# Kernel tuning notes

Measured on AMD Instinct MI355X. Metric: run time of the kernel, lower is better.

The kernel has to match this reference:

```python
import math
import jax, jax.numpy as jnp
import numpy as np

B, T_ALL, D = 128, 197, 768
T = T_ALL - 1
ORG, E, DFF, NCLS = 5, 8, 1024, 100
CAP_FACTOR = 1.25
MAX_K = 2  # training=True -> min(2, n_experts)


def setup_inputs() -> dict:
    key = jax.random.key(0)
    ks = jax.random.split(key, 16)
    s = lambda *sh: 0.02
    inp = {
        "tokens": jax.random.normal(ks[0], (B, T_ALL, D), jnp.float32),
        "organ_priors": jax.random.uniform(ks[1], (B, ORG), jnp.float32),
        "router_w": jax.random.normal(ks[2], (D + ORG, E), jnp.float32) * 0.02,
        "router_b": jnp.zeros((E,), jnp.float32),
        "w1": jax.random.normal(ks[3], (E, D, DFF), jnp.float32) * 0.02,
        "b1": jnp.zeros((E, DFF), jnp.float32),
        "w2": jax.random.normal(ks[4], (E, DFF, D), jnp.float32) * 0.02,
        "b2": jnp.zeros((E, D), jnp.float32),
        "ln_g": jnp.ones((D,), jnp.float32),
        "ln_b": jnp.zeros((D,), jnp.float32),
        "cls_w": jax.random.normal(ks[5], (D, NCLS), jnp.float32) * 0.02,
        "cls_b": jnp.zeros((NCLS,), jnp.float32),
        "aux_w": jax.random.normal(ks[6], (D, ORG), jnp.float32) * 0.02,
        "aux_b": jnp.zeros((ORG,), jnp.float32),
    }
    return inp


def switch_moe(flat, flat_prior, router_w, router_b, w1, b1, w2, b2):
    N = flat.shape[0]
    capacity = math.ceil(N / E * CAP_FACTOR)  # static
    logits = jnp.concatenate([flat, flat_prior], axis=-1) @ router_w + router_b  # (N,E)
    probs = jax.nn.softmax(logits, axis=-1)
    entropy = -(probs * jnp.log(probs + 1e-12)).sum(-1)  # (N,)
    topk_vals, topk_idx = jax.lax.top_k(probs, MAX_K)  # (N,K)
    topk_probs = topk_vals / (topk_vals.sum(-1, keepdims=True) + 1e-12)
    # one-hot expert assignment over top-k slots: (N,E)
    sel = jnp.any(topk_idx[:, None, :] == jnp.arange(E)[None, :, None], axis=-1)
    # combine weight per (token, expert): first (unique) matching top-k slot's prob
    w_full = (topk_probs[:, None, :] * (topk_idx[:, None, :] == jnp.arange(E)[None, :, None])).sum(-1)  # (N,E)
    # capacity-limited dispatch: per expert keep top-`capacity` tokens by router prob
    score = jnp.where(sel, probs, -jnp.inf).T  # (E,N)
    top_scores, idx = jax.lax.top_k(score, capacity)  # (E,cap), sorted desc like torch.sort
    valid = jnp.isfinite(top_scores)  # (E,cap)
    gathered = flat[idx]  # (E,cap,D)
    h = jax.nn.gelu(jnp.einsum('ecd,edf->ecf', gathered, w1) + b1[:, None, :], approximate=False)
    out_sel = jnp.einsum('ecf,efd->ecd', h, w2) + b2[:, None, :]  # (E,cap,D)
    w_sel = jnp.take_along_axis(w_full.T, idx, axis=1) * valid  # (E,cap)
    flat_idx = idx.reshape(-1)
    outputs = jnp.zeros_like(flat).at[flat_idx].add((out_sel * w_sel[..., None]).reshape(-1, D))
    processed = jnp.zeros((N,), jnp.float32).at[flat_idx].add(valid.reshape(-1).astype(jnp.float32)) > 0
    outputs = jnp.where(processed[:, None], outputs, flat)
    return outputs, probs, entropy


def reference(tokens, organ_priors, router_w, router_b, w1, b1, w2, b2,
              ln_g, ln_b, cls_w, cls_b, aux_w, aux_b):
    cls = tokens[:, 0, :]                # (B,D)
    patches = tokens[:, 1:, :]           # (B,T,D)
    flat = patches.reshape(B * T, D)
    flat_prior = jnp.broadcast_to(organ_priors[:, None, :], (B, T, ORG)).reshape(B * T, ORG)
    out_flat, probs, entropy = switch_moe(flat, flat_prior, router_w, router_b, w1, b1, w2, b2)
    # cls token passes through MoE untouched (only patches go through switch)
    mu = cls.mean(-1, keepdims=True)
    var = ((cls - mu) ** 2).mean(-1, keepdims=True)
    cls_final = (cls - mu) * jax.lax.rsqrt(var + 1e-5) * ln_g + ln_b
    logits = cls_final @ cls_w + cls_b
    aux_org = cls_final @ aux_w + aux_b
    return logits, aux_org, probs.reshape(B, T, E), entropy.reshape(B, T)
```

## Files before the change

kernel.cpp:

```cpp
#include <hip/hip_runtime.h>
#include <hip/hip_bf16.h>
#include <math.h>

#define NB     128
#define NT_ALL 197
#define NT     196
#define ND     768
#define NORG   5
#define NE     8
#define NCLS   100
#define NCOL   105
#define NTOK   (NB * NT)
#define KB     24

#define CBLKS  256
#define RBLKS  392

typedef short  bf16x8 __attribute__((ext_vector_type(8)));
typedef float  f32x4  __attribute__((ext_vector_type(4)));


__global__ __launch_bounds__(256, 4) void fused_kernel(
    const float* __restrict__ tokens,
    const float* __restrict__ priors,
    const float* __restrict__ rw,
    const float* __restrict__ rbias,
    const float* __restrict__ ln_g, const float* __restrict__ ln_b,
    const float* __restrict__ cls_w,
    const float* __restrict__ cls_b,
    const float* __restrict__ aux_w,
    const float* __restrict__ aux_b,
    float* __restrict__ out_logits,
    float* __restrict__ out_aux,
    float* __restrict__ probs_out,
    float* __restrict__ ent_out)
{
    const int t = threadIdx.x;

    if (blockIdx.x >= CBLKS) {
        const int rblk = blockIdx.x - CBLKS;

        __shared__ __align__(16) __hip_bfloat16 s_a[KB * 4 * 16 * 8];
        __shared__ float s_pl[2][NE];

        {
            bf16x8 z = {0, 0, 0, 0, 0, 0, 0, 0};
            bf16x8* p = (bf16x8*)s_a;
            for (int i = t; i < KB * 4 * 16; i += 256) p[i] = z;
        }
        __syncthreads();

        for (int i = t; i < ND * NE; i += 256) {
            const int k = i >> 3, e = i & 7;
            const int kb = k >> 5, g = (k >> 3) & 3, j = k & 7;
            s_a[(((kb * 4 + g) * 16) + e) * 8 + j] = __float2bfloat16(rw[i]);
        }

        const int tok0 = rblk * 64;
        const int b0 = tok0 / NT;
        const int b1 = (tok0 + 63) / NT;
        if (t < 16) {
            const int e = t & 7, which = t >> 3;
            const int b = which ? b1 : b0;
            float a = rbias[e];
#pragma unroll
            for (int o = 0; o < NORG; ++o)
                a = fmaf(priors[b * NORG + o], rw[(ND + o) * NE + e], a);
            s_pl[which][e] = a;
        }
        __syncthreads();

        const int wid  = t >> 6;
        const int lane = t & 63;
        const int gbase = tok0 + wid * 16;
        const int tt = lane & 15;
        const int g  = lane >> 4;
        const int token = gbase + tt;
        const int b  = token / NT;
        const float* xp = tokens + ((size_t)b * NT_ALL + 1 + (token - b * NT)) * ND
                          + g * 8;

        const bf16x8* s_a8 = (const bf16x8*)s_a;
        f32x4 acc = {0.f, 0.f, 0.f, 0.f};

#pragma unroll 8
        for (int kb = 0; kb < KB; ++kb) {
            const float4 x0 = *reinterpret_cast<const float4*>(xp + kb * 32);
            const float4 x1 = *reinterpret_cast<const float4*>(xp + kb * 32 + 4);
            union { bf16x8 v; __hip_bfloat16 h[8]; } u;
            u.h[0] = __float2bfloat16(x0.x);
            u.h[1] = __float2bfloat16(x0.y);
            u.h[2] = __float2bfloat16(x0.z);
            u.h[3] = __float2bfloat16(x0.w);
            u.h[4] = __float2bfloat16(x1.x);
            u.h[5] = __float2bfloat16(x1.y);
            u.h[6] = __float2bfloat16(x1.z);
            u.h[7] = __float2bfloat16(x1.w);
            const bf16x8 af = s_a8[(kb * 4 + g) * 16 + tt];
            acc = __builtin_amdgcn_mfma_f32_16x16x32_bf16(af, u.v, acc, 0, 0, 0);
        }

        const float p0 = __shfl_xor(acc[0], 16, 64);
        const float p1 = __shfl_xor(acc[1], 16, 64);
        const float p2 = __shfl_xor(acc[2], 16, 64);
        const float p3 = __shfl_xor(acc[3], 16, 64);

        if (lane < 16) {
            float lg[NE] = {acc[0], acc[1], acc[2], acc[3], p0, p1, p2, p3};
            const int bsel = (token >= (b0 + 1) * NT) ? 1 : 0;
#pragma unroll
            for (int e = 0; e < NE; ++e) lg[e] += s_pl[bsel][e];

            float m = lg[0];
#pragma unroll
            for (int e = 1; e < NE; ++e) m = fmaxf(m, lg[e]);
            float S = 0.f, dd = 0.f;
#pragma unroll
            for (int e = 0; e < NE; ++e) {
                const float l = lg[e] - m;
                const float p = __expf(l);
                lg[e] = p;
                S += p;
                dd = fmaf(p, l, dd);
            }
            const float inv = 1.f / S;
            const float ent = __logf(S) - dd * inv;

            float4 q0 = {lg[0] * inv, lg[1] * inv, lg[2] * inv, lg[3] * inv};
            float4 q1 = {lg[4] * inv, lg[5] * inv, lg[6] * inv, lg[7] * inv};
            *reinterpret_cast<float4*>(probs_out + (size_t)token * NE)     = q0;
            *reinterpret_cast<float4*>(probs_out + (size_t)token * NE + 4) = q1;
            ent_out[token] = ent;
        }
    } else {
        const int cb   = blockIdx.x;
        const int b    = cb >> 1;
        const int half = cb & 1;
        const int lane = t & 63;
        const int wv   = t >> 6;

        __shared__ __align__(16) float s_x[ND];
        __shared__ float s_red[4];
        __shared__ float s_part[4][65];

        const float* xp = tokens + (size_t)b * NT_ALL * ND;

        float sum = 0.f;
        for (int i = t; i < ND; i += 256) { float v = xp[i]; s_x[i] = v; sum += v; }
#pragma unroll
        for (int off = 32; off; off >>= 1) sum += __shfl_xor(sum, off, 64);
        if (lane == 0) s_red[wv] = sum;
        __syncthreads();
        const float mu = (s_red[0] + s_red[1] + s_red[2] + s_red[3]) * (1.f / ND);
        __syncthreads();

        float sq = 0.f;
        for (int i = t; i < ND; i += 256) { float d = s_x[i] - mu; sq += d * d; }
#pragma unroll
        for (int off = 32; off; off >>= 1) sq += __shfl_xor(sq, off, 64);
        if (lane == 0) s_red[wv] = sq;
        __syncthreads();
        const float var  = (s_red[0] + s_red[1] + s_red[2] + s_red[3]) * (1.f / ND);
        const float rstd = rsqrtf(var + 1e-5f);
        __syncthreads();

        for (int i = t; i < ND; i += 256)
            s_x[i] = (s_x[i] - mu) * rstd * ln_g[i] + ln_b[i];
        __syncthreads();

        const int c = half * 64 + lane;
        const float* wp; int st;
        if (c < NCLS)      { wp = cls_w + c;          st = NCLS; }
        else if (c < NCOL) { wp = aux_w + (c - NCLS); st = NORG; }
        else               { wp = aux_w;              st = NORG; }

        const int d0 = wv * 192;
        const float* w = wp + (size_t)d0 * st;
        const int st2 = 2 * st, st3 = 3 * st, st4 = 4 * st;
        float a0 = 0.f, a1 = 0.f, a2 = 0.f, a3 = 0.f;
#pragma unroll 8
        for (int j = 0; j < 192; j += 4) {
            const float4 x4 = *reinterpret_cast<const float4*>(&s_x[d0 + j]);
            a0 = fmaf(x4.x, w[0],   a0);
            a1 = fmaf(x4.y, w[st],  a1);
            a2 = fmaf(x4.z, w[st2], a2);
            a3 = fmaf(x4.w, w[st3], a3);
            w += st4;
        }
        s_part[wv][lane] = (a0 + a1) + (a2 + a3);
        __syncthreads();

        if (t < 64) {
            float r = s_part[0][t] + s_part[1][t] + s_part[2][t] + s_part[3][t];
            const int cc = half * 64 + t;
            if (cc < NCLS)
                out_logits[b * NCLS + cc] = r + cls_b[cc];
            else if (cc < NCOL)
                out_aux[b * NORG + (cc - NCLS)] = r + aux_b[cc - NCLS];
        }
    }
}

extern "C" void kernel_launch(void* const* d_in, const int* in_sizes, int n_in,
                              void* d_out, int out_size, void* d_ws, size_t ws_size,
                              hipStream_t stream) {
    const float* tokens = (const float*)d_in[0];
    const float* priors = (const float*)d_in[1];
    const float* rw     = (const float*)d_in[2];
    const float* rbias  = (const float*)d_in[3];
    const float* ln_g   = (const float*)d_in[8];
    const float* ln_b   = (const float*)d_in[9];
    const float* cls_w  = (const float*)d_in[10];
    const float* cls_b  = (const float*)d_in[11];
    const float* aux_w  = (const float*)d_in[12];
    const float* aux_b  = (const float*)d_in[13];

    float* out = (float*)d_out;
    float* out_logits = out;
    float* out_aux    = out + NB * NCLS;
    float* out_probs  = out + NB * NCLS + NB * NORG;
    float* out_ent    = out + NB * NCLS + NB * NORG + (size_t)NTOK * NE;

    fused_kernel<<<CBLKS + RBLKS, 256, 0, stream>>>(
        tokens, priors, rw, rbias, ln_g, ln_b, cls_w, cls_b, aux_w, aux_b,
        out_logits, out_aux, out_probs, out_ent);
}
```

Before: 26.23 us.

## Prefetch token loads before router weight staging and split MFMA accumulators

```diff
diff --git a/kernel.cpp b/kernel.cpp
--- a/kernel.cpp
+++ b/kernel.cpp
@@ -12,6 +12,7 @@
 #define NCOL   105
 #define NTOK   (NB * NT)
 #define KB     24
+#define PF     6
 
 #define CBLKS  256
 #define RBLKS  392
@@ -43,35 +44,9 @@
         __shared__ __align__(16) __hip_bfloat16 s_a[KB * 4 * 16 * 8];
         __shared__ float s_pl[2][NE];
 
-        {
-            bf16x8 z = {0, 0, 0, 0, 0, 0, 0, 0};
-            bf16x8* p = (bf16x8*)s_a;
-            for (int i = t; i < KB * 4 * 16; i += 256) p[i] = z;
-        }
-        __syncthreads();
-
-        for (int i = t; i < ND * NE; i += 256) {
-            const int k = i >> 3, e = i & 7;
-            const int kb = k >> 5, g = (k >> 3) & 3, j = k & 7;
-            s_a[(((kb * 4 + g) * 16) + e) * 8 + j] = __float2bfloat16(rw[i]);
-        }
-
-        const int tok0 = rblk * 64;
-        const int b0 = tok0 / NT;
-        const int b1 = (tok0 + 63) / NT;
-        if (t < 16) {
-            const int e = t & 7, which = t >> 3;
-            const int b = which ? b1 : b0;
-            float a = rbias[e];
-#pragma unroll
-            for (int o = 0; o < NORG; ++o)
-                a = fmaf(priors[b * NORG + o], rw[(ND + o) * NE + e], a);
-            s_pl[which][e] = a;
-        }
-        __syncthreads();
-
         const int wid  = t >> 6;
         const int lane = t & 63;
+        const int tok0 = rblk * 64;
         const int gbase = tok0 + wid * 16;
         const int tt = lane & 15;
         const int g  = lane >> 4;
@@ -80,13 +55,45 @@
         const float* xp = tokens + ((size_t)b * NT_ALL + 1 + (token - b * NT)) * ND
                           + g * 8;
 
+        float4 xb[PF][2];
+#pragma unroll
+        for (int i = 0; i < PF; ++i) {
+            xb[i][0] = *reinterpret_cast<const float4*>(xp + i * 32);
+            xb[i][1] = *reinterpret_cast<const float4*>(xp + i * 32 + 4);
+        }
+
+        {
+            bf16x8 z = {0, 0, 0, 0, 0, 0, 0, 0};
+            bf16x8* p = (bf16x8*)s_a;
+            for (int i = t; i < KB * 4 * 8; i += 256)
+                p[(i >> 3) * 16 + 8 + (i & 7)] = z;
+        }
+        for (int i = t; i < ND * NE; i += 256) {
+            const int k = i >> 3, e = i & 7;
+            const int kb = k >> 5, gg = (k >> 3) & 3, j = k & 7;
+            s_a[(((kb * 4 + gg) * 16) + e) * 8 + j] = __float2bfloat16(rw[i]);
+        }
+        const int b0 = tok0 / NT;
+        const int b1 = (tok0 + 63) / NT;
+        if (t < 16) {
+            const int e = t & 7, which = t >> 3;
+            const int bb = which ? b1 : b0;
+            float a = rbias[e];
+#pragma unroll
+            for (int o = 0; o < NORG; ++o)
+                a = fmaf(priors[bb * NORG + o], rw[(ND + o) * NE + e], a);
+            s_pl[which][e] = a;
+        }
+        __syncthreads();
+
         const bf16x8* s_a8 = (const bf16x8*)s_a;
-        f32x4 acc = {0.f, 0.f, 0.f, 0.f};
-
-#pragma unroll 8
+        f32x4 acc0 = {0.f, 0.f, 0.f, 0.f};
+        f32x4 acc1 = {0.f, 0.f, 0.f, 0.f};
+
+#pragma unroll
         for (int kb = 0; kb < KB; ++kb) {
-            const float4 x0 = *reinterpret_cast<const float4*>(xp + kb * 32);
-            const float4 x1 = *reinterpret_cast<const float4*>(xp + kb * 32 + 4);
+            const float4 x0 = xb[kb % PF][0];
+            const float4 x1 = xb[kb % PF][1];
             union { bf16x8 v; __hip_bfloat16 h[8]; } u;
             u.h[0] = __float2bfloat16(x0.x);
             u.h[1] = __float2bfloat16(x0.y);
@@ -97,8 +104,16 @@
             u.h[6] = __float2bfloat16(x1.z);
             u.h[7] = __float2bfloat16(x1.w);
             const bf16x8 af = s_a8[(kb * 4 + g) * 16 + tt];
-            acc = __builtin_amdgcn_mfma_f32_16x16x32_bf16(af, u.v, acc, 0, 0, 0);
-        }
+            if (kb & 1)
+                acc1 = __builtin_amdgcn_mfma_f32_16x16x32_bf16(af, u.v, acc1, 0, 0, 0);
+            else
+                acc0 = __builtin_amdgcn_mfma_f32_16x16x32_bf16(af, u.v, acc0, 0, 0, 0);
+            if (kb + PF < KB) {
+                xb[kb % PF][0] = *reinterpret_cast<const float4*>(xp + (kb + PF) * 32);
+                xb[kb % PF][1] = *reinterpret_cast<const float4*>(xp + (kb + PF) * 32 + 4);
+            }
+        }
+        const f32x4 acc = acc0 + acc1;
 
         const float p0 = __shfl_xor(acc[0], 16, 64);
         const float p1 = __shfl_xor(acc[1], 16, 64);
```

Result: no change. 25.96 us (-1.0%).
